# Performance work log

Hardware: AMD Instinct MI355X
Metric: run time of the kernel (lower is better)

Reference implementation:

```python
import jax, jax.numpy as jnp
import numpy as np

DIM = 768
HEADS = 12
HEAD_DIM = DIM // HEADS
EPS = 1e-12  # torch F.normalize eps


def setup_inputs() -> dict:
    key = jax.random.key(0)
    k1, k2, k3 = jax.random.split(key, 3)
    x = jax.random.normal(k1, (8, 4096, DIM), dtype=jnp.float32)
    # qkv: Linear(dim, 3*dim, bias=False); proj: Linear(dim, dim) with bias
    s = 1.0 / np.sqrt(DIM)
    w_qkv = jax.random.uniform(k2, (3 * DIM, DIM), dtype=jnp.float32, minval=-s, maxval=s)
    w_proj = jax.random.uniform(k3, (DIM, DIM), dtype=jnp.float32, minval=-s, maxval=s)
    b_proj = jnp.zeros((DIM,), dtype=jnp.float32)
    return {"x": x, "w_qkv": w_qkv, "w_proj": w_proj, "b_proj": b_proj}


def _l1_normalize(t):
    # normalize over token axis N (axis=-2), matching F.normalize(p=1, dim=-2)
    denom = jnp.maximum(jnp.sum(jnp.abs(t), axis=-2, keepdims=True), EPS)
    return t / denom


def reference(x, w_qkv, w_proj, b_proj):
    B, N, C = x.shape
    hd = C // HEADS
    qkv = x @ w_qkv.T  # [B, N, 3C]
    qkv = qkv.reshape(B, N, 3, HEADS, hd).transpose(2, 0, 3, 1, 4)  # [3, B, H, N, hd]
    q, k, v = qkv[0], qkv[1], qkv[2]
    q = _l1_normalize(q)
    k = _l1_normalize(k)
    if N < hd:
        out = jnp.einsum('bhnd,bhmd,bhme->bhne', q, k, v)
    else:
        kv = jnp.einsum('bhnd,bhne->bhde', k, v)  # [B, H, hd, hd]
        out = jnp.einsum('bhnd,bhde->bhne', q, kv)  # [B, H, N, hd]
    out = out.transpose(0, 2, 1, 3).reshape(B, N, C)
    return out @ w_proj.T + b_proj
```

## Files before the change

### kernel.cpp

```cpp
#include <hip/hip_runtime.h>
#include <cstddef>
#include <cstdint>

#define DIMC   768
#define HEADS  12
#define HD     64
#define BATCH  8
#define SEQ    4096
#define MTOK   (BATCH*SEQ)
#define THREEC (3*DIMC)
#define BHN    (BATCH*HEADS)
#define NCHUNK 8
#define CHTOK  (SEQ/NCHUNK)
#define EPSN   1e-12f
#define KT     (DIMC/32)
#define TILE_U16 1024
#define ROWTILE_U16 (KT*TILE_U16)

typedef unsigned short u16;
typedef unsigned int   u32;
typedef __attribute__((ext_vector_type(8))) short short8;
typedef __attribute__((ext_vector_type(4))) float f32x4;

__device__ inline u16 bf16_rne(float f) {
  u32 u = __float_as_uint(f);
  u32 r = u + 0x7fffu + ((u >> 16) & 1u);
  return (u16)(r >> 16);
}

__device__ inline u32 cvt_pk_bf16(float a, float b) {
  u32 r;
  asm("v_cvt_pk_bf16_f32 %0, %1, %2" : "=v"(r) : "v"(a), "v"(b));
  return r;
}

__global__ __launch_bounds__(256)
void split_tiles(const float* __restrict__ in, u16* __restrict__ outp,
                 int nrowtiles) {
  const int l = threadIdx.x & 63;
  const int ntiles = nrowtiles * KT;
  for (int gw = (blockIdx.x * 256 + threadIdx.x) >> 6; gw < ntiles;
       gw += (gridDim.x * 256) >> 6) {
    const int rt = gw / KT, kt = gw % KT;
    const float* src = in + (size_t)(rt * 16 + (l & 15)) * DIMC + kt * 32 + (l >> 4) * 8;
    float4 x0 = *(const float4*)src;
    float4 x1 = *(const float4*)(src + 4);
    float xs[8] = {x0.x, x0.y, x0.z, x0.w, x1.x, x1.y, x1.z, x1.w};
    u32 hw[4], lw[4];
    #pragma unroll
    for (int i = 0; i < 4; ++i) {
      u16 h0 = bf16_rne(xs[2*i]);
      u16 h1 = bf16_rne(xs[2*i+1]);
      float r0 = xs[2*i]   - __uint_as_float(((u32)h0) << 16);
      float r1 = xs[2*i+1] - __uint_as_float(((u32)h1) << 16);
      u16 l0 = bf16_rne(r0);
      u16 l1 = bf16_rne(r1);
      hw[i] = (u32)h0 | ((u32)h1 << 16);
      lw[i] = (u32)l0 | ((u32)l1 << 16);
    }
    u16* tb = outp + (size_t)gw * TILE_U16;
    *(uint4*)(tb + l * 8)       = make_uint4(hw[0], hw[1], hw[2], hw[3]);
    *(uint4*)(tb + 512 + l * 8) = make_uint4(lw[0], lw[1], lw[2], lw[3]);
  }
}

__global__ __launch_bounds__(256)
void split_tiles_t(const float* __restrict__ in, u16* __restrict__ outp,
                   int nrowtiles, int ld) {
  const int l = threadIdx.x & 63;
  const int ntiles = nrowtiles * KT;
  for (int gw = (blockIdx.x * 256 + threadIdx.x) >> 6; gw < ntiles;
       gw += (gridDim.x * 256) >> 6) {
    const int rt = gw / KT, kt = gw % KT;
    const int m = rt * 16 + (l & 15);
    const int k0 = kt * 32 + (l >> 4) * 8;
    float xs[8];
    #pragma unroll
    for (int j = 0; j < 8; ++j) xs[j] = in[(size_t)(k0 + j) * ld + m];
    u32 hw[4], lw[4];
    #pragma unroll
    for (int i = 0; i < 4; ++i) {
      u16 h0 = bf16_rne(xs[2*i]);
      u16 h1 = bf16_rne(xs[2*i+1]);
      float r0 = xs[2*i]   - __uint_as_float(((u32)h0) << 16);
      float r1 = xs[2*i+1] - __uint_as_float(((u32)h1) << 16);
      u16 l0 = bf16_rne(r0);
      u16 l1 = bf16_rne(r1);
      hw[i] = (u32)h0 | ((u32)h1 << 16);
      lw[i] = (u32)l0 | ((u32)l1 << 16);
    }
    u16* tb = outp + (size_t)gw * TILE_U16;
    *(uint4*)(tb + l * 8)       = make_uint4(hw[0], hw[1], hw[2], hw[3]);
    *(uint4*)(tb + 512 + l * 8) = make_uint4(lw[0], lw[1], lw[2], lw[3]);
  }
}

__global__ __launch_bounds__(256, 3)
void qkv_stage1(const u16* __restrict__ xc, const u16* __restrict__ wc,
                float* __restrict__ kvp, float* __restrict__ dqp,
                float* __restrict__ dkp) {
  const int bid = blockIdx.x;
  const int h = bid % HEADS;
  const int bc = bid / HEADS;
  const int b = bc >> 3, chunk = bc & 7;
  const int bh = b * HEADS + h;
  const int si = bh * NCHUNK + chunk;

  const int tid = threadIdx.x;
  const int w = tid >> 6, l = tid & 63;
  const int lr16 = l & 15, cg = l >> 4;

  __shared__ __align__(16) unsigned char smem[33792];
  u16* lds16 = (u16*)smem;
  float* red = (float*)smem;

  f32x4 kvacc[4] = {(f32x4){0,0,0,0},(f32x4){0,0,0,0},(f32x4){0,0,0,0},(f32x4){0,0,0,0}};
  float dsum_q = 0.f, dsum_k = 0.f;

  const u16* wbase[3];
  #pragma unroll
  for (int ot = 0; ot < 3; ++ot) {
    const int grow = ot * DIMC + h * HD + w * 16;
    wbase[ot] = wc + (size_t)(grow >> 4) * ROWTILE_U16 + (l << 3);
  }
  const int atile0 = (b * SEQ + chunk * CHTOK) >> 4;

  for (int sub = 0; sub < 8; ++sub) {
    const u16* asub = xc + (size_t)(atile0 + sub * 4) * ROWTILE_U16;
    __syncthreads();
    {
      const u16* g = asub + (size_t)w * ROWTILE_U16 + (l << 3);
      uint4 s0 = *(const uint4*)g;
      uint4 s1 = *(const uint4*)(g + 512);
      *(uint4*)(lds16 + w * 1024 + (l << 3))       = s0;
      *(uint4*)(lds16 + w * 1024 + 512 + (l << 3)) = s1;
    }
    __syncthreads();

    f32x4 acc[4][3];
    #pragma unroll
    for (int tt = 0; tt < 4; ++tt)
      #pragma unroll
      for (int ot = 0; ot < 3; ++ot)
        acc[tt][ot] = (f32x4){0.f, 0.f, 0.f, 0.f};

    for (int kt = 0; kt < KT; ++kt) {
      const int cur = (kt & 1) << 12;
      const int nxt = cur ^ 4096;
      uint4 s0, s1;
      if (kt + 1 < KT) {
        const u16* g = asub + (size_t)w * ROWTILE_U16 + (kt + 1) * TILE_U16 + (l << 3);
        s0 = *(const uint4*)g;
        s1 = *(const uint4*)(g + 512);
      }
      const int off = kt * TILE_U16;
      short8 bh_[3], bl_[3];
      #pragma unroll
      for (int ot = 0; ot < 3; ++ot) {
        bh_[ot] = *(const short8*)(wbase[ot] + off);
        bl_[ot] = *(const short8*)(wbase[ot] + off + 512);
      }
      #pragma unroll
      for (int tt = 0; tt < 4; ++tt) {
        short8 ah = *(const short8*)(lds16 + cur + tt * 1024 + (l << 3));
        short8 al = *(const short8*)(lds16 + cur + tt * 1024 + 512 + (l << 3));
        #pragma unroll
        for (int ot = 0; ot < 3; ++ot) {
          acc[tt][ot] = __builtin_amdgcn_mfma_f32_16x16x32_bf16(ah, bh_[ot], acc[tt][ot], 0, 0, 0);
          acc[tt][ot] = __builtin_amdgcn_mfma_f32_16x16x32_bf16(ah, bl_[ot], acc[tt][ot], 0, 0, 0);
          acc[tt][ot] = __builtin_amdgcn_mfma_f32_16x16x32_bf16(al, bh_[ot], acc[tt][ot], 0, 0, 0);
        }
      }
      if (kt + 1 < KT) {
        *(uint4*)(lds16 + nxt + w * 1024 + (l << 3))       = s0;
        *(uint4*)(lds16 + nxt + w * 1024 + 512 + (l << 3)) = s1;
      }
      __syncthreads();
    }
    #pragma unroll
    for (int tt = 0; tt < 4; ++tt) {
      dsum_q += fabsf(acc[tt][0][0]);
      dsum_q += fabsf(acc[tt][0][1]);
      dsum_q += fabsf(acc[tt][0][2]);
      dsum_q += fabsf(acc[tt][0][3]);
    }
    #pragma unroll
    for (int sec = 1; sec < 3; ++sec) {
      const int region = (sec == 1) ? 0 : 8192;
      #pragma unroll
      for (int tt = 0; tt < 4; ++tt) {
        const float v0 = acc[tt][sec][0], v1 = acc[tt][sec][1];
        const float v2 = acc[tt][sec][2], v3 = acc[tt][sec][3];
        if (sec == 1) {
          dsum_k += fabsf(v0);
          dsum_k += fabsf(v1);
          dsum_k += fabsf(v2);
          dsum_k += fabsf(v3);
        }
        const u32 ph01 = cvt_pk_bf16(v0, v1);
        const u32 ph23 = cvt_pk_bf16(v2, v3);
        const float r0 = v0 - __uint_as_float(ph01 << 16);
        const float r1 = v1 - __uint_as_float(ph01 & 0xffff0000u);
        const float r2 = v2 - __uint_as_float(ph23 << 16);
        const float r3 = v3 - __uint_as_float(ph23 & 0xffff0000u);
        const u32 pl01 = cvt_pk_bf16(r0, r1);
        const u32 pl23 = cvt_pk_bf16(r2, r3);
        const int pos = region + (w * 2 + (tt >> 1)) * TILE_U16 +
                        ((lr16 | (((tt * 2 + (cg >> 1)) & 3) << 4)) << 3) +
                        ((cg & 1) << 2);
        *(uint2*)(lds16 + pos)       = make_uint2(ph01, ph23);
        *(uint2*)(lds16 + pos + 512) = make_uint2(pl01, pl23);
      }
    }
    __syncthreads();
    {
      const u16* At = lds16 + w * 2 * TILE_U16;
      const u16* Bt = lds16 + 8192;
      #pragma unroll
      for (int t2 = 0; t2 < 2; ++t2) {
        short8 kah = *(const short8*)(At + t2 * TILE_U16 + (l << 3));
        short8 kal = *(const short8*)(At + t2 * TILE_U16 + 512 + (l << 3));
        #pragma unroll
        for (int et = 0; et < 4; ++et) {
          short8 vbh = *(const short8*)(Bt + (et * 2 + t2) * TILE_U16 + (l << 3));
          short8 vbl = *(const short8*)(Bt + (et * 2 + t2) * TILE_U16 + 512 + (l << 3));
          kvacc[et] = __builtin_amdgcn_mfma_f32_16x16x32_bf16(kah, vbh, kvacc[et], 0, 0, 0);
          kvacc[et] = __builtin_amdgcn_mfma_f32_16x16x32_bf16(kah, vbl, kvacc[et], 0, 0, 0);
          kvacc[et] = __builtin_amdgcn_mfma_f32_16x16x32_bf16(kal, vbh, kvacc[et], 0, 0, 0);
        }
      }
    }
  }
  float* ob = kvp + (size_t)si * (HD * HD);
  #pragma unroll
  for (int et = 0; et < 4; ++et)
    #pragma unroll
    for (int r = 0; r < 4; ++r)
      ob[(w * 16 + cg * 4 + r) * HD + et * 16 + lr16] = kvacc[et][r];
  __syncthreads();
  red[(w * 16 + lr16) * 4 + cg]       = dsum_q;
  red[256 + (w * 16 + lr16) * 4 + cg] = dsum_k;
  __syncthreads();
  if (tid < 64) {
    dqp[(size_t)si * HD + tid] = red[tid*4] + red[tid*4+1] + red[tid*4+2] + red[tid*4+3];
  } else if (tid < 128) {
    const int d = tid - 64;
    dkp[(size_t)si * HD + d] = red[256 + d*4] + red[256 + d*4+1] + red[256 + d*4+2] + red[256 + d*4+3];
  }
}

__global__ __launch_bounds__(256)
void kv_reduce(const float* __restrict__ kvp, const float* __restrict__ dqp,
               const float* __restrict__ dkp, float* __restrict__ kvs) {
  const int bh = blockIdx.x;
  const int tid = threadIdx.x;
  __shared__ float dqL[64], dkL[64];
  if (tid < 64) {
    float s = 0.f;
    #pragma unroll
    for (int c = 0; c < NCHUNK; ++c) s += dqp[((size_t)bh * NCHUNK + c) * HD + tid];
    dqL[tid] = fmaxf(s, EPSN);
  } else if (tid < 128) {
    const int d = tid - 64;
    float s = 0.f;
    #pragma unroll
    for (int c = 0; c < NCHUNK; ++c) s += dkp[((size_t)bh * NCHUNK + c) * HD + d];
    dkL[d] = fmaxf(s, EPSN);
  }
  __syncthreads();
  #pragma unroll
  for (int i = 0; i < 16; ++i) {
    const int idx = i * 256 + tid;
    const int d = idx >> 6;
    float s = 0.f;
    #pragma unroll
    for (int c = 0; c < NCHUNK; ++c)
      s += kvp[((size_t)bh * NCHUNK + c) * (HD * HD) + idx];
    kvs[(size_t)bh * (HD * HD) + idx] = s / (dqL[d] * dkL[d]);
  }
}

__global__ __launch_bounds__(256)
void w2_kernel(const float* __restrict__ kvs, const float* __restrict__ w_proj,
               float* __restrict__ W2T) {
  const int bh = blockIdx.x;
  const int b = bh / HEADS, h = bh % HEADS;
  const int c0 = blockIdx.y * 128;
  const int tid = threadIdx.x;
  const int tx = tid & 15, ty = tid >> 4;
  __shared__ float KVe[64][68];
  __shared__ float Wp[64][132];
  #pragma unroll
  for (int i = 0; i < 4; ++i) {
    const int idx = i * 256 + tid;
    const int d  = idx >> 4;
    const int e4 = (idx & 15) << 2;
    float4 v4 = *(const float4*)&kvs[(size_t)bh * (HD*HD) + (size_t)d * HD + e4];
    KVe[e4+0][d] = v4.x; KVe[e4+1][d] = v4.y;
    KVe[e4+2][d] = v4.z; KVe[e4+3][d] = v4.w;
  }
  {
    const int c = tid >> 1, half = tid & 1;
    #pragma unroll
    for (int j = 0; j < 8; ++j) {
      const int e = half * 32 + j * 4;
      float4 v4 = *(const float4*)&w_proj[(size_t)(c0 + c) * DIMC + h * HD + e];
      Wp[e+0][c] = v4.x; Wp[e+1][c] = v4.y; Wp[e+2][c] = v4.z; Wp[e+3][c] = v4.w;
    }
  }
  __syncthreads();
  float acc[4][8] = {};
  for (int e = 0; e < 64; ++e) {
    float4 a4 = *(const float4*)&KVe[e][ty << 2];
    float4 b0 = *(const float4*)&Wp[e][tx << 3];
    float4 b1 = *(const float4*)&Wp[e][(tx << 3) + 4];
    float ar[4] = {a4.x, a4.y, a4.z, a4.w};
    float br[8] = {b0.x,b0.y,b0.z,b0.w,b1.x,b1.y,b1.z,b1.w};
    #pragma unroll
    for (int i = 0; i < 4; ++i)
      #pragma unroll
      for (int j = 0; j < 8; ++j)
        acc[i][j] = fmaf(ar[i], br[j], acc[i][j]);
  }
  float* W2Tb = W2T + (size_t)b * DIMC * DIMC;
  #pragma unroll
  for (int j = 0; j < 8; ++j)
    *(float4*)&W2Tb[(size_t)(c0 + (tx << 3) + j) * DIMC + h * HD + (ty << 2)] =
        make_float4(acc[0][j], acc[1][j], acc[2][j], acc[3][j]);
}

__global__ __launch_bounds__(256)
void w3t_mfma(const u16* __restrict__ w2c, const u16* __restrict__ wqt,
              float* __restrict__ W3T) {
  const int tid = threadIdx.x;
  const int w = tid >> 6, l = tid & 63;
  const int lr16 = l & 15, cg = l >> 4;
  const int cx = blockIdx.x, my = blockIdx.y, b = blockIdx.z;

  const u16* wbase[3];
  #pragma unroll
  for (int ot = 0; ot < 3; ++ot)
    wbase[ot] = wqt + (size_t)(my * 12 + w * 3 + ot) * ROWTILE_U16 + (l << 3);
  const u16* abase[4];
  #pragma unroll
  for (int tt = 0; tt < 4; ++tt)
    abase[tt] = w2c + (size_t)(b * 48 + cx * 4 + tt) * ROWTILE_U16 + (l << 3);

  f32x4 acc[4][3];
  #pragma unroll
  for (int tt = 0; tt < 4; ++tt)
    #pragma unroll
    for (int ot = 0; ot < 3; ++ot)
      acc[tt][ot] = (f32x4){0.f, 0.f, 0.f, 0.f};

  for (int kt = 0; kt < KT; ++kt) {
    const int off = kt * TILE_U16;
    short8 bh_[3], bl_[3];
    #pragma unroll
    for (int ot = 0; ot < 3; ++ot) {
      bh_[ot] = *(const short8*)(wbase[ot] + off);
      bl_[ot] = *(const short8*)(wbase[ot] + off + 512);
    }
    #pragma unroll
    for (int tt = 0; tt < 4; ++tt) {
      short8 ah = *(const short8*)(abase[tt] + off);
      short8 al = *(const short8*)(abase[tt] + off + 512);
      #pragma unroll
      for (int ot = 0; ot < 3; ++ot) {
        acc[tt][ot] = __builtin_amdgcn_mfma_f32_16x16x32_bf16(ah, bh_[ot], acc[tt][ot], 0, 0, 0);
        acc[tt][ot] = __builtin_amdgcn_mfma_f32_16x16x32_bf16(ah, bl_[ot], acc[tt][ot], 0, 0, 0);
        acc[tt][ot] = __builtin_amdgcn_mfma_f32_16x16x32_bf16(al, bh_[ot], acc[tt][ot], 0, 0, 0);
      }
    }
  }
  float* Wb = W3T + (size_t)b * DIMC * DIMC;
  #pragma unroll
  for (int ot = 0; ot < 3; ++ot) {
    const int col = my * 192 + w * 48 + ot * 16 + lr16;
    #pragma unroll
    for (int tt = 0; tt < 4; ++tt) {
      const int row0 = cx * 64 + tt * 16 + cg * 4;
      #pragma unroll
      for (int r = 0; r < 4; ++r)
        Wb[(size_t)(row0 + r) * DIMC + col] = acc[tt][ot][r];
    }
  }
}

__global__ __launch_bounds__(256, 3)
void final_gemm_mfma(const u16* __restrict__ xc, const u16* __restrict__ w3c,
                     const float* __restrict__ bias, float* __restrict__ out) {
  const int tid = threadIdx.x;
  const int w = tid >> 6, l = tid & 63;
  const int lr16 = l & 15, cg = l >> 4;
  const int ntile = blockIdx.x;
  const int c0 = blockIdx.y * 192;
  const int b = ntile >> 6;
  const int colbase0 = c0 + w * 48;

  const u16* wbase[3];
  #pragma unroll
  for (int ot = 0; ot < 3; ++ot) {
    const int c = colbase0 + ot * 16;
    wbase[ot] = w3c + (size_t)(b * (DIMC/16) + (c >> 4)) * ROWTILE_U16 + (l << 3);
  }
  const u16* abase[4];
  #pragma unroll
  for (int tt = 0; tt < 4; ++tt)
    abase[tt] = xc + (size_t)(ntile * 4 + tt) * ROWTILE_U16 + (l << 3);

  f32x4 acc[4][3];
  #pragma unroll
  for (int tt = 0; tt < 4; ++tt)
    #pragma unroll
    for (int ot = 0; ot < 3; ++ot)
      acc[tt][ot] = (f32x4){0.f, 0.f, 0.f, 0.f};

  for (int kt = 0; kt < KT; ++kt) {
    const int off = kt * TILE_U16;
    short8 bh_[3], bl_[3];
    #pragma unroll
    for (int ot = 0; ot < 3; ++ot) {
      bh_[ot] = *(const short8*)(wbase[ot] + off);
      bl_[ot] = *(const short8*)(wbase[ot] + off + 512);
    }
    #pragma unroll
    for (int tt = 0; tt < 4; ++tt) {
      short8 ah = *(const short8*)(abase[tt] + off);
      short8 al = *(const short8*)(abase[tt] + off + 512);
      #pragma unroll
      for (int ot = 0; ot < 3; ++ot) {
        acc[tt][ot] = __builtin_amdgcn_mfma_f32_16x16x32_bf16(ah, bh_[ot], acc[tt][ot], 0, 0, 0);
        acc[tt][ot] = __builtin_amdgcn_mfma_f32_16x16x32_bf16(ah, bl_[ot], acc[tt][ot], 0, 0, 0);
        acc[tt][ot] = __builtin_amdgcn_mfma_f32_16x16x32_bf16(al, bh_[ot], acc[tt][ot], 0, 0, 0);
      }
    }
  }
  #pragma unroll
  for (int ot = 0; ot < 3; ++ot) {
    const int col = colbase0 + ot * 16 + lr16;
    const float bv = bias[col];
    #pragma unroll
    for (int tt = 0; tt < 4; ++tt) {
      const size_t row0 = (size_t)ntile * 64 + tt * 16 + cg * 4;
      #pragma unroll
      for (int r = 0; r < 4; ++r)
        out[(row0 + r) * DIMC + col] = acc[tt][ot][r] + bv;
    }
  }
}

extern "C" void kernel_launch(void* const* d_in, const int* in_sizes, int n_in,
                              void* d_out, int out_size, void* d_ws, size_t ws_size,
                              hipStream_t stream) {
  const float* x      = (const float*)d_in[0];
  const float* w_qkv  = (const float*)d_in[1];
  const float* w_proj = (const float*)d_in[2];
  const float* b_proj = (const float*)d_in[3];
  float* out = (float*)d_out;
  float* ws  = (float*)d_ws;

  const size_t KVP_SZ = (size_t)BHN * NCHUNK * HD * HD;
  const size_t DQP_SZ = (size_t)BHN * NCHUNK * HD;
  const size_t KVS_SZ = (size_t)BHN * HD * HD;
  const size_t W_SZ   = (size_t)BATCH * DIMC * DIMC;
  const size_t XC_U16  = (size_t)(MTOK/16) * ROWTILE_U16;
  const size_t WC_U16  = (size_t)(THREEC/16) * ROWTILE_U16;
  const size_t WQT_U16 = (size_t)(DIMC/16) * ROWTILE_U16;
  const size_t W2C_U16 = (size_t)(BATCH*DIMC/16) * ROWTILE_U16;
  const size_t W3C_U16 = (size_t)(BATCH*DIMC/16) * ROWTILE_U16;
  float* kvp  = ws;
  float* dqp  = kvp + KVP_SZ;
  float* dkp  = dqp + DQP_SZ;
  float* kvs  = dkp + DQP_SZ;
  float* WBUF = kvs + KVS_SZ;
  u16*   xc   = (u16*)(WBUF + W_SZ);
  u16*   wc   = xc + XC_U16;
  u16*   wqt  = wc + WC_U16;
  u16*   w2c  = wqt + WQT_U16;
  u16*   w3c  = w2c + W2C_U16;
  const size_t need_bytes =
      (KVP_SZ + 2*DQP_SZ + KVS_SZ + W_SZ) * sizeof(float) +
      (XC_U16 + WC_U16 + WQT_U16 + W2C_U16 + W3C_U16) * sizeof(u16);
  if (ws_size < need_bytes) return;

  const dim3 blk(256);
  split_tiles<<<dim3((MTOK/16) * KT / 4), blk, 0, stream>>>(x, xc, MTOK/16);
  split_tiles<<<dim3((THREEC/16) * KT / 4), blk, 0, stream>>>(w_qkv, wc, THREEC/16);
  split_tiles_t<<<dim3((DIMC/16) * KT / 4), blk, 0, stream>>>(w_qkv, wqt, DIMC/16, DIMC);
  qkv_stage1<<<dim3(BHN * NCHUNK), blk, 0, stream>>>(xc, wc, kvp, dqp, dkp);
  kv_reduce<<<dim3(BHN), blk, 0, stream>>>(kvp, dqp, dkp, kvs);
  w2_kernel<<<dim3(BHN, DIMC/128), blk, 0, stream>>>(kvs, w_proj, WBUF);
  split_tiles<<<dim3((BATCH*DIMC/16) * KT / 4), blk, 0, stream>>>(WBUF, w2c, BATCH*DIMC/16);
  w3t_mfma<<<dim3(DIMC/64, DIMC/192, BATCH), blk, 0, stream>>>(w2c, wqt, WBUF);
  split_tiles<<<dim3((BATCH*DIMC/16) * KT / 4), blk, 0, stream>>>(WBUF, w3c, BATCH*DIMC/16);
  final_gemm_mfma<<<dim3(MTOK/64, DIMC/192), blk, 0, stream>>>(xc, w3c, b_proj, out);
}
```

Baseline: 547.5 us.

## Stage final GEMM A tiles through double-buffered LDS and add MFMA priority hints

```diff
diff --git a/kernel.cpp b/kernel.cpp
--- a/kernel.cpp
+++ b/kernel.cpp
@@ -127,11 +127,11 @@
 
   for (int sub = 0; sub < 8; ++sub) {
     const u16* asub = xc + (size_t)(atile0 + sub * 4) * ROWTILE_U16;
+    const u16* gw0 = asub + (size_t)w * ROWTILE_U16 + (l << 3);
     __syncthreads();
     {
-      const u16* g = asub + (size_t)w * ROWTILE_U16 + (l << 3);
-      uint4 s0 = *(const uint4*)g;
-      uint4 s1 = *(const uint4*)(g + 512);
+      uint4 s0 = *(const uint4*)gw0;
+      uint4 s1 = *(const uint4*)(gw0 + 512);
       *(uint4*)(lds16 + w * 1024 + (l << 3))       = s0;
       *(uint4*)(lds16 + w * 1024 + 512 + (l << 3)) = s1;
     }
@@ -149,7 +149,7 @@
       const int nxt = cur ^ 4096;
       uint4 s0, s1;
       if (kt + 1 < KT) {
-        const u16* g = asub + (size_t)w * ROWTILE_U16 + (kt + 1) * TILE_U16 + (l << 3);
+        const u16* g = gw0 + (kt + 1) * TILE_U16;
         s0 = *(const uint4*)g;
         s1 = *(const uint4*)(g + 512);
       }
@@ -160,6 +160,7 @@
         bh_[ot] = *(const short8*)(wbase[ot] + off);
         bl_[ot] = *(const short8*)(wbase[ot] + off + 512);
       }
+      __builtin_amdgcn_s_setprio(1);
       #pragma unroll
       for (int tt = 0; tt < 4; ++tt) {
         short8 ah = *(const short8*)(lds16 + cur + tt * 1024 + (l << 3));
@@ -171,6 +172,7 @@
           acc[tt][ot] = __builtin_amdgcn_mfma_f32_16x16x32_bf16(al, bh_[ot], acc[tt][ot], 0, 0, 0);
         }
       }
+      __builtin_amdgcn_s_setprio(0);
       if (kt + 1 < KT) {
         *(uint4*)(lds16 + nxt + w * 1024 + (l << 3))       = s0;
         *(uint4*)(lds16 + nxt + w * 1024 + 512 + (l << 3)) = s1;
@@ -216,6 +218,7 @@
     {
       const u16* At = lds16 + w * 2 * TILE_U16;
       const u16* Bt = lds16 + 8192;
+      __builtin_amdgcn_s_setprio(1);
       #pragma unroll
       for (int t2 = 0; t2 < 2; ++t2) {
         short8 kah = *(const short8*)(At + t2 * TILE_U16 + (l << 3));
@@ -229,6 +232,7 @@
           kvacc[et] = __builtin_amdgcn_mfma_f32_16x16x32_bf16(kal, vbh, kvacc[et], 0, 0, 0);
         }
       }
+      __builtin_amdgcn_s_setprio(0);
     }
   }
   float* ob = kvp + (size_t)si * (HD * HD);
@@ -398,16 +402,23 @@
   const int b = ntile >> 6;
   const int colbase0 = c0 + w * 48;
 
+  __shared__ __align__(16) u16 alds[8192];
+
   const u16* wbase[3];
   #pragma unroll
   for (int ot = 0; ot < 3; ++ot) {
     const int c = colbase0 + ot * 16;
     wbase[ot] = w3c + (size_t)(b * (DIMC/16) + (c >> 4)) * ROWTILE_U16 + (l << 3);
   }
-  const u16* abase[4];
-  #pragma unroll
-  for (int tt = 0; tt < 4; ++tt)
-    abase[tt] = xc + (size_t)(ntile * 4 + tt) * ROWTILE_U16 + (l << 3);
+  const u16* gw0 = xc + (size_t)(ntile * 4 + w) * ROWTILE_U16 + (l << 3);
+
+  {
+    uint4 a0 = *(const uint4*)gw0;
+    uint4 a1 = *(const uint4*)(gw0 + 512);
+    *(uint4*)(alds + w * 1024 + (l << 3))       = a0;
+    *(uint4*)(alds + w * 1024 + 512 + (l << 3)) = a1;
+  }
+  __syncthreads();
 
   f32x4 acc[4][3];
   #pragma unroll
@@ -417,6 +428,14 @@
       acc[tt][ot] = (f32x4){0.f, 0.f, 0.f, 0.f};
 
   for (int kt = 0; kt < KT; ++kt) {
+    const int cur = (kt & 1) << 12;
+    const int nxt = cur ^ 4096;
+    uint4 s0, s1;
+    if (kt + 1 < KT) {
+      const u16* g = gw0 + (kt + 1) * TILE_U16;
+      s0 = *(const uint4*)g;
+      s1 = *(const uint4*)(g + 512);
+    }
     const int off = kt * TILE_U16;
     short8 bh_[3], bl_[3];
     #pragma unroll
@@ -424,10 +443,11 @@
       bh_[ot] = *(const short8*)(wbase[ot] + off);
       bl_[ot] = *(const short8*)(wbase[ot] + off + 512);
     }
+    __builtin_amdgcn_s_setprio(1);
     #pragma unroll
     for (int tt = 0; tt < 4; ++tt) {
-      short8 ah = *(const short8*)(abase[tt] + off);
-      short8 al = *(const short8*)(abase[tt] + off + 512);
+      short8 ah = *(const short8*)(alds + cur + tt * 1024 + (l << 3));
+      short8 al = *(const short8*)(alds + cur + tt * 1024 + 512 + (l << 3));
       #pragma unroll
       for (int ot = 0; ot < 3; ++ot) {
         acc[tt][ot] = __builtin_amdgcn_mfma_f32_16x16x32_bf16(ah, bh_[ot], acc[tt][ot], 0, 0, 0);
@@ -435,6 +455,12 @@
         acc[tt][ot] = __builtin_amdgcn_mfma_f32_16x16x32_bf16(al, bh_[ot], acc[tt][ot], 0, 0, 0);
       }
     }
+    __builtin_amdgcn_s_setprio(0);
+    if (kt + 1 < KT) {
+      *(uint4*)(alds + nxt + w * 1024 + (l << 3))       = s0;
+      *(uint4*)(alds + nxt + w * 1024 + 512 + (l << 3)) = s1;
+    }
+    __syncthreads();
   }
   #pragma unroll
   for (int ot = 0; ot < 3; ++ot) {
```

Measured after the change: 523.1 us. 1.05x faster.
